# Kernel tuning notes

Measured on AMD Instinct MI355X. Metric: run time of the kernel, lower is better.

## Reference

```python
import jax, jax.numpy as jnp
import numpy as np

N_NODES = 50000

def setup_inputs() -> dict:
    key = jax.random.key(0)
    ks = jax.random.split(key, 4)
    x = jax.random.normal(ks[0], (N_NODES, 64), dtype=jnp.float32)
    edge_index = jax.random.randint(ks[1], (2, 800000), 0, N_NODES, dtype=jnp.int64)
    W1 = jax.random.normal(ks[2], (64, 128), dtype=jnp.float32) * (1.0 / np.sqrt(64))
    b1 = jnp.zeros((128,), dtype=jnp.float32)
    W2 = jax.random.normal(ks[3], (128, 64), dtype=jnp.float32) * (1.0 / np.sqrt(128))
    b2 = jnp.zeros((64,), dtype=jnp.float32)
    eps = jnp.zeros((1,), dtype=jnp.float32)
    return {"x": x, "edge_index": edge_index, "W1": W1, "b1": b1, "W2": W2, "b2": b2, "eps": eps}

def reference(x, edge_index, W1, b1, W2, b2, eps):
    row, col = edge_index[0], edge_index[1]
    # gather neighbor features [E, d] and scatter-add into destination nodes [N, d]
    agg = jax.ops.segment_sum(x[col], row, num_segments=x.shape[0])
    h = (1.0 + eps[0]) * x + agg
    # 2-layer MLP: Linear -> ReLU -> Linear
    h = jax.nn.relu(h @ W1 + b1)
    return h @ W2 + b2
```

## Files before the change

### kernel.cpp

```cpp
#include <hip/hip_runtime.h>

#define N_NODES 50000
#define N_EDGES 800000
#define D 64
#define H 128
#define NB512 128
#define NLIVE 98
#define CAP 9216
#define BT 2048
#define NBB 391
#define TILE2 2304
#define NSUB 32
#define SCAP2 352
#define CVB 798

typedef __attribute__((ext_vector_type(8))) short  short8;
typedef __attribute__((ext_vector_type(4))) float  floatx4;
typedef __attribute__((ext_vector_type(4))) unsigned short ushort4v;

__device__ inline unsigned short f2bf(float f) {
    unsigned u = __builtin_bit_cast(unsigned, f);
    u += 0x7FFFu + ((u >> 16) & 1u);
    return (unsigned short)(u >> 16);
}
__device__ inline float bf2f(unsigned short b) {
    unsigned u = (unsigned)b << 16;
    return __builtin_bit_cast(float, u);
}

__global__ __launch_bounds__(1024) void bin_prep(
    const int* __restrict__ row, const int* __restrict__ col,
    int* __restrict__ cursor, int* __restrict__ csr,
    const float* __restrict__ x, unsigned short* __restrict__ xb,
    const float* __restrict__ W1, unsigned short* __restrict__ w1t,
    const float* __restrict__ W2, unsigned short* __restrict__ w2t)
{
    int t = threadIdx.x;
    if (blockIdx.x >= NBB) {
        int tid = (blockIdx.x - NBB) * 1024 + t;
        if (tid < 800000) {
            float4 v = ((const float4*)x)[tid];
            ushort4v o;
            o.x = f2bf(v.x); o.y = f2bf(v.y); o.z = f2bf(v.z); o.w = f2bf(v.w);
            ((ushort4v*)xb)[tid] = o;
        } else {
            int i = tid - 800000;
            if (i < D * H) {
                int k = i >> 7, n = i & 127;
                w1t[n * D + k] = f2bf(W1[i]);
            } else if (i < 2 * D * H) {
                int j = i - D * H;
                int k = j >> 6, n = j & 63;
                w2t[n * H + k] = f2bf(W2[j]);
            }
        }
        return;
    }

    __shared__ int cnt[NB512];
    __shared__ int loffs[NB512];
    __shared__ int gbase[NB512];
    __shared__ int sorted[BT];
    __shared__ int wsum[2];

    int lane = t & 63;
    if (t < NB512) cnt[t] = 0;
    __syncthreads();

    int base = blockIdx.x * BT;
    int ia = base + t, ib = ia + 1024;
    int ca = min(ia, N_EDGES - 1), cb = min(ib, N_EDGES - 1);
    unsigned ra = (unsigned)row[ca], rb = (unsigned)row[cb];
    unsigned ka = (unsigned)col[ca], kb = (unsigned)col[cb];
    bool va = ia < N_EDGES, vb = ib < N_EDGES;
    if (va) atomicAdd(&cnt[ra >> 9], 1);
    if (vb) atomicAdd(&cnt[rb >> 9], 1);
    __syncthreads();

    int v = 0, incl = 0;
    if (t < NB512) {
        v = cnt[t];
        incl = v;
        #pragma unroll
        for (int d = 1; d < 64; d <<= 1) {
            int y = __shfl_up(incl, d);
            if (lane >= d) incl += y;
        }
        if (lane == 63) wsum[t >> 6] = incl;
    }
    __syncthreads();
    if (t < NB512) {
        int add = (t >= 64) ? wsum[0] : 0;
        loffs[t] = incl - v + add;
        if (v) gbase[t] = t * CAP + atomicAdd(&cursor[t], v);
    }
    __syncthreads();

    if (t < NB512) cnt[t] = 0;
    __syncthreads();

    if (va) { int b = (int)(ra >> 9); int lp = atomicAdd(&cnt[b], 1);
              sorted[loffs[b] + lp] = (int)((ra << 16) | ka); }
    if (vb) { int b = (int)(rb >> 9); int lp = atomicAdd(&cnt[b], 1);
              sorted[loffs[b] + lp] = (int)((rb << 16) | kb); }
    __syncthreads();

    int nloc = min(BT, N_EDGES - base);
    for (int i = t; i < nloc; i += 1024) {
        unsigned en = (unsigned)sorted[i];
        int b = (int)(en >> 25);
        int pos = gbase[b] + (i - loffs[b]);
        csr[pos] = (int)en;
    }
}

__global__ __launch_bounds__(256) void subsort(
    const int* __restrict__ cursor, const int* __restrict__ csr,
    int* __restrict__ cursor2, int* __restrict__ csr2)
{
    __shared__ int sorted[TILE2];
    __shared__ int cnt32[32], loffs[32], gbase[32], curs[32];

    int t = threadIdx.x, lane = t & 63;
    int bucket = blockIdx.x >> 2;
    int tile   = blockIdx.x & 3;

    int cntE = min(cursor[bucket], CAP);
    int tbeg = tile * TILE2;
    int nloc = max(min(tbeg + TILE2, cntE) - tbeg, 0);
    const int* src = csr + bucket * CAP + tbeg;

    if (t < 32) cnt32[t] = 0;
    __syncthreads();

    for (int i = t; i < nloc; i += 256)
        atomicAdd(&cnt32[(((unsigned)src[i] >> 16) & 511u) >> 4], 1);
    __syncthreads();

    if (t < 32) {
        int v = cnt32[t];
        int incl = v;
        #pragma unroll
        for (int d = 1; d < 32; d <<= 1) {
            int y = __shfl_up(incl, d);
            if (lane >= d) incl += y;
        }
        loffs[t] = incl - v;
        curs[t]  = incl - v;
        gbase[t] = v ? atomicAdd(&cursor2[bucket * 32 + t], v) : 0;
    }
    __syncthreads();

    for (int i = t; i < nloc; i += 256) {
        unsigned e = (unsigned)src[i];
        int local = (int)((e >> 16) & 511u);
        int p = atomicAdd(&curs[local >> 4], 1);
        sorted[p] = (int)(((unsigned)local << 16) | (e & 0xFFFFu));
    }
    __syncthreads();

    for (int i = t; i < nloc; i += 256) {
        unsigned en = (unsigned)sorted[i];
        int sub = (int)(en >> 20);
        int rel = gbase[sub] + (i - loffs[sub]);
        if (rel < SCAP2)
            csr2[(bucket * 32 + sub) * SCAP2 + rel] =
                (int)(((en >> 16) & 15u) << 16 | (en & 0xFFFFu));
    }
}

__global__ __launch_bounds__(256, 8) void gather_mlp(
    const float* __restrict__ x, const unsigned short* __restrict__ xb,
    const int* __restrict__ cursor2, const int* __restrict__ csr2,
    const unsigned short* __restrict__ w1t, const float* __restrict__ b1,
    const unsigned short* __restrict__ w2t, const float* __restrict__ b2,
    const float* __restrict__ eps, float* __restrict__ out)
{
    __shared__ int ent[SCAP2];
    __shared__ unsigned short scol[SCAP2];
    __shared__ int cnt16[16], offs[17], curs[16];
    __shared__ unsigned short HB[16][72];
    __shared__ unsigned short HID[16][136];

    int t = threadIdx.x, lane = t & 63, wid = t >> 6;
    int bs = blockIdx.x;
    int bucket = bs >> 5, sub = bs & 31;

    if (t < 16) cnt16[t] = 0;
    __syncthreads();

    int n2 = min(cursor2[bs], SCAP2);
    const int* src = csr2 + (size_t)bs * SCAP2;

    for (int i = t; i < n2; i += 256) {
        int e = src[i];
        ent[i] = e;
        atomicAdd(&cnt16[((unsigned)e >> 16) & 15u], 1);
    }
    __syncthreads();

    if (t < 16) {
        int v = cnt16[t];
        int incl = v;
        #pragma unroll
        for (int d = 1; d < 16; d <<= 1) {
            int y = __shfl_up(incl, d);
            if (lane >= d) incl += y;
        }
        offs[t] = incl - v;
        curs[t] = incl - v;
        if (t == 15) offs[16] = incl;
    }
    __syncthreads();

    for (int i = t; i < n2; i += 256) {
        int e = ent[i];
        int nl = (int)(((unsigned)e >> 16) & 15u);
        int p = atomicAdd(&curs[nl], 1);
        scol[p] = (unsigned short)(e & 0xFFFF);
    }
    __syncthreads();

    float ep = 1.0f + eps[0];
    int half = lane >> 5, fl = lane & 31;
    #pragma unroll 1
    for (int nn = 0; nn < 4; ++nn) {
        int nl = wid * 4 + nn;
        int node = bucket * 512 + sub * 16 + nl;
        int jb = offs[nl], je = offs[nl + 1];
        float s0a = 0.f, s1a = 0.f, s0b = 0.f, s1b = 0.f;
        float s0c = 0.f, s1c = 0.f, s0d = 0.f, s1d = 0.f;
        int j = jb;
        for (; j + 8 <= je; j += 8) {
            int c0 = scol[j + half];
            int c1 = scol[j + 2 + half];
            int c2 = scol[j + 4 + half];
            int c3 = scol[j + 6 + half];
            ushort2 p0 = *(const ushort2*)&xb[c0 * D + 2 * fl];
            ushort2 p1 = *(const ushort2*)&xb[c1 * D + 2 * fl];
            ushort2 p2 = *(const ushort2*)&xb[c2 * D + 2 * fl];
            ushort2 p3 = *(const ushort2*)&xb[c3 * D + 2 * fl];
            s0a += bf2f(p0.x); s1a += bf2f(p0.y);
            s0b += bf2f(p1.x); s1b += bf2f(p1.y);
            s0c += bf2f(p2.x); s1c += bf2f(p2.y);
            s0d += bf2f(p3.x); s1d += bf2f(p3.y);
        }
        for (; j < je; j += 2) {
            if (j + half < je) {
                int c = scol[j + half];
                ushort2 p = *(const ushort2*)&xb[c * D + 2 * fl];
                s0a += bf2f(p.x); s1a += bf2f(p.y);
            }
        }
        float s0 = (s0a + s0b) + (s0c + s0d);
        float s1 = (s1a + s1b) + (s1c + s1d);
        s0 += __shfl_xor(s0, 32);
        s1 += __shfl_xor(s1, 32);
        if (half == 0) {
            float2 xv = {0.f, 0.f};
            if (node < N_NODES) xv = *(const float2*)&x[(size_t)node * D + 2 * fl];
            ushort2 o;
            o.x = f2bf(fmaf(ep, xv.x, s0));
            o.y = f2bf(fmaf(ep, xv.y, s1));
            *(ushort2*)&HB[nl][2 * fl] = o;
        }
    }
    __syncthreads();

    if (wid == 0) {
        int m = lane & 15, q = lane >> 4;
        short8 a0 = *(const short8*)&HB[m][q * 8];
        short8 a1 = *(const short8*)&HB[m][32 + q * 8];

        #pragma unroll
        for (int nt = 0; nt < 8; ++nt) {
            float bias = b1[nt * 16 + m];
            floatx4 acc = {bias, bias, bias, bias};
            short8 w0 = *(const short8*)&w1t[(nt * 16 + m) * D + q * 8];
            short8 w1 = *(const short8*)&w1t[(nt * 16 + m) * D + 32 + q * 8];
            acc = __builtin_amdgcn_mfma_f32_16x16x32_bf16(a0, w0, acc, 0, 0, 0);
            acc = __builtin_amdgcn_mfma_f32_16x16x32_bf16(a1, w1, acc, 0, 0, 0);
            #pragma unroll
            for (int r = 0; r < 4; ++r) {
                float hv = fmaxf(acc[r], 0.0f);
                HID[q * 4 + r][nt * 16 + m] = f2bf(hv);
            }
        }

        short8 ha[4];
        #pragma unroll
        for (int kc2 = 0; kc2 < 4; ++kc2)
            ha[kc2] = *(const short8*)&HID[m][kc2 * 32 + q * 8];

        #pragma unroll
        for (int nt2 = 0; nt2 < 4; ++nt2) {
            float bias = b2[nt2 * 16 + m];
            floatx4 acc = {bias, bias, bias, bias};
            #pragma unroll
            for (int kc2 = 0; kc2 < 4; ++kc2) {
                short8 w = *(const short8*)&w2t[(nt2 * 16 + m) * H + kc2 * 32 + q * 8];
                acc = __builtin_amdgcn_mfma_f32_16x16x32_bf16(ha[kc2], w, acc, 0, 0, 0);
            }
            #pragma unroll
            for (int r = 0; r < 4; ++r) {
                int nn2 = bucket * 512 + sub * 16 + q * 4 + r;
                if (nn2 < N_NODES) out[(size_t)nn2 * D + nt2 * 16 + m] = acc[r];
            }
        }
    }
}

extern "C" void kernel_launch(void* const* d_in, const int* in_sizes, int n_in,
                              void* d_out, int out_size, void* d_ws, size_t ws_size,
                              hipStream_t stream) {
    const float* x   = (const float*)d_in[0];
    const int*   ei  = (const int*)  d_in[1];
    const float* W1  = (const float*)d_in[2];
    const float* b1  = (const float*)d_in[3];
    const float* W2  = (const float*)d_in[4];
    const float* b2  = (const float*)d_in[5];
    const float* eps = (const float*)d_in[6];
    float* out = (float*)d_out;

    unsigned short* xb  = (unsigned short*)d_ws;
    unsigned short* w1t = xb + (size_t)N_NODES * D;
    unsigned short* w2t = w1t + D * H;
    int* csr     = (int*)(w2t + D * H);
    int* csr2    = csr + (size_t)NB512 * CAP;
    int* cursor  = csr2 + (size_t)NLIVE * 32 * SCAP2;
    int* cursor2 = cursor + NB512;

    const int* row = ei;
    const int* col = ei + N_EDGES;

    hipMemsetAsync(cursor, 0, (size_t)(NB512 + NLIVE * 32) * sizeof(int), stream);
    bin_prep<<<NBB + CVB, 1024, 0, stream>>>(row, col, cursor, csr,
                                             x, xb, W1, w1t, W2, w2t);
    subsort<<<NLIVE * 4, 256, 0, stream>>>(cursor, csr, cursor2, csr2);
    gather_mlp<<<NLIVE * 32, 256, 0, stream>>>(x, xb, cursor2, csr2,
                                               w1t, b1, w2t, b2, eps, out);
}
```

Measured before the change: 128.0 us.

## Replace global bucket atomics with per-tile fixed-slot bins and drop memset

The first binning pass no longer reserves space with global atomics on per-bucket cursors. Each input tile now writes its edges into a fixed-capacity slot per bucket (52 entries) and records per-tile counts. The subsort kernel gathers these slots for its bucket across 49 tiles, and runs with 8 blocks per bucket instead of 4. The cursor2 zeroing moves into bin_prep, removing the separate memset launch. The cost is a strided, sparse gather in subsort and silent truncation if any tile/bucket pair exceeds its slot capacity.

```diff
diff --git a/kernel.cpp b/kernel.cpp
--- a/kernel.cpp
+++ b/kernel.cpp
@@ -4,13 +4,13 @@
 #define N_EDGES 800000
 #define D 64
 #define H 128
-#define NB512 128
 #define NLIVE 98
-#define CAP 9216
+#define NBPAD 128
 #define BT 2048
 #define NBB 391
-#define TILE2 2304
-#define NSUB 32
+#define CAPT 52
+#define NT8 49
+#define STG 1280
 #define SCAP2 352
 #define CVB 798
 
@@ -30,14 +30,18 @@
 
 __global__ __launch_bounds__(1024) void bin_prep(
     const int* __restrict__ row, const int* __restrict__ col,
-    int* __restrict__ cursor, int* __restrict__ csr,
+    int* __restrict__ counts, int* __restrict__ csr,
+    int* __restrict__ cursor2,
     const float* __restrict__ x, unsigned short* __restrict__ xb,
     const float* __restrict__ W1, unsigned short* __restrict__ w1t,
     const float* __restrict__ W2, unsigned short* __restrict__ w2t)
 {
     int t = threadIdx.x;
     if (blockIdx.x >= NBB) {
-        int tid = (blockIdx.x - NBB) * 1024 + t;
+        int cb = blockIdx.x - NBB;
+        if (cb == 0)
+            for (int i = t; i < NLIVE * 32; i += 1024) cursor2[i] = 0;
+        int tid = cb * 1024 + t;
         if (tid < 800000) {
             float4 v = ((const float4*)x)[tid];
             ushort4v o;
@@ -57,28 +61,27 @@
         return;
     }
 
-    __shared__ int cnt[NB512];
-    __shared__ int loffs[NB512];
-    __shared__ int gbase[NB512];
+    __shared__ int cnt[NBPAD];
+    __shared__ int loffs[NBPAD];
     __shared__ int sorted[BT];
     __shared__ int wsum[2];
 
     int lane = t & 63;
-    if (t < NB512) cnt[t] = 0;
+    if (t < NBPAD) cnt[t] = 0;
     __syncthreads();
 
     int base = blockIdx.x * BT;
     int ia = base + t, ib = ia + 1024;
-    int ca = min(ia, N_EDGES - 1), cb = min(ib, N_EDGES - 1);
-    unsigned ra = (unsigned)row[ca], rb = (unsigned)row[cb];
-    unsigned ka = (unsigned)col[ca], kb = (unsigned)col[cb];
+    int ca = min(ia, N_EDGES - 1), cb2 = min(ib, N_EDGES - 1);
+    unsigned ra = (unsigned)row[ca], rb = (unsigned)row[cb2];
+    unsigned ka = (unsigned)col[ca], kb = (unsigned)col[cb2];
     bool va = ia < N_EDGES, vb = ib < N_EDGES;
     if (va) atomicAdd(&cnt[ra >> 9], 1);
     if (vb) atomicAdd(&cnt[rb >> 9], 1);
     __syncthreads();
 
     int v = 0, incl = 0;
-    if (t < NB512) {
+    if (t < NBPAD) {
         v = cnt[t];
         incl = v;
         #pragma unroll
@@ -89,14 +92,13 @@
         if (lane == 63) wsum[t >> 6] = incl;
     }
     __syncthreads();
-    if (t < NB512) {
-        int add = (t >= 64) ? wsum[0] : 0;
-        loffs[t] = incl - v + add;
-        if (v) gbase[t] = t * CAP + atomicAdd(&cursor[t], v);
-    }
-    __syncthreads();
-
-    if (t < NB512) cnt[t] = 0;
+    if (t < NBPAD) {
+        loffs[t] = incl - v + ((t >= 64) ? wsum[0] : 0);
+        if (t < NLIVE) counts[blockIdx.x * NLIVE + t] = min(v, CAPT);
+    }
+    __syncthreads();
+
+    if (t < NBPAD) cnt[t] = 0;
     __syncthreads();
 
     if (va) { int b = (int)(ra >> 9); int lp = atomicAdd(&cnt[b], 1);
@@ -109,34 +111,44 @@
     for (int i = t; i < nloc; i += 1024) {
         unsigned en = (unsigned)sorted[i];
         int b = (int)(en >> 25);
-        int pos = gbase[b] + (i - loffs[b]);
-        csr[pos] = (int)en;
-    }
-}
-
-__global__ __launch_bounds__(256) void subsort(
-    const int* __restrict__ cursor, const int* __restrict__ csr,
+        int rel = i - loffs[b];
+        if (rel < CAPT)
+            csr[((size_t)blockIdx.x * NLIVE + b) * CAPT + rel] = (int)en;
+    }
+}
+
+__global__ __launch_bounds__(256, 8) void subsort(
+    const int* __restrict__ counts, const int* __restrict__ csr,
     int* __restrict__ cursor2, int* __restrict__ csr2)
 {
-    __shared__ int sorted[TILE2];
+    __shared__ int tcnt[NT8];
+    __shared__ int stage[STG];
+    __shared__ int sorted2[STG];
     __shared__ int cnt32[32], loffs[32], gbase[32], curs[32];
+    __shared__ int nstage;
 
     int t = threadIdx.x, lane = t & 63;
-    int bucket = blockIdx.x >> 2;
-    int tile   = blockIdx.x & 3;
-
-    int cntE = min(cursor[bucket], CAP);
-    int tbeg = tile * TILE2;
-    int nloc = max(min(tbeg + TILE2, cntE) - tbeg, 0);
-    const int* src = csr + bucket * CAP + tbeg;
+    int bucket = blockIdx.x >> 3, q = blockIdx.x & 7;
+    int tbeg = q * NT8;
+    int ntile = min(NT8, NBB - tbeg);
 
     if (t < 32) cnt32[t] = 0;
-    __syncthreads();
-
-    for (int i = t; i < nloc; i += 256)
-        atomicAdd(&cnt32[(((unsigned)src[i] >> 16) & 511u) >> 4], 1);
-    __syncthreads();
-
+    if (t == 0) nstage = 0;
+    if (t < ntile) tcnt[t] = counts[(size_t)(tbeg + t) * NLIVE + bucket];
+    __syncthreads();
+
+    for (int s = t; s < ntile * CAPT; s += 256) {
+        int tl = s / CAPT, slot = s - tl * CAPT;
+        if (slot < tcnt[tl]) {
+            int e = csr[((size_t)(tbeg + tl) * NLIVE + bucket) * CAPT + slot];
+            int p = atomicAdd(&nstage, 1);
+            stage[min(p, STG - 1)] = e;
+            atomicAdd(&cnt32[((unsigned)e >> 20) & 31u], 1);
+        }
+    }
+    __syncthreads();
+
+    int nst = min(nstage, STG);
     if (t < 32) {
         int v = cnt32[t];
         int incl = v;
@@ -151,21 +163,21 @@
     }
     __syncthreads();
 
-    for (int i = t; i < nloc; i += 256) {
-        unsigned e = (unsigned)src[i];
-        int local = (int)((e >> 16) & 511u);
-        int p = atomicAdd(&curs[local >> 4], 1);
-        sorted[p] = (int)(((unsigned)local << 16) | (e & 0xFFFFu));
-    }
-    __syncthreads();
-
-    for (int i = t; i < nloc; i += 256) {
-        unsigned en = (unsigned)sorted[i];
-        int sub = (int)(en >> 20);
+    for (int i = t; i < nst; i += 256) {
+        int e = stage[i];
+        int sub = (int)(((unsigned)e >> 20) & 31u);
+        int p = atomicAdd(&curs[sub], 1);
+        sorted2[min(p, STG - 1)] = e;
+    }
+    __syncthreads();
+
+    for (int i = t; i < nst; i += 256) {
+        unsigned en = (unsigned)sorted2[i];
+        int sub = (int)((en >> 20) & 31u);
         int rel = gbase[sub] + (i - loffs[sub]);
         if (rel < SCAP2)
-            csr2[(bucket * 32 + sub) * SCAP2 + rel] =
-                (int)(((en >> 16) & 15u) << 16 | (en & 0xFFFFu));
+            csr2[((size_t)bucket * 32 + sub) * SCAP2 + rel] =
+                (int)(en & 0xFFFFFu);
     }
 }
 
@@ -326,17 +338,16 @@
     unsigned short* w1t = xb + (size_t)N_NODES * D;
     unsigned short* w2t = w1t + D * H;
     int* csr     = (int*)(w2t + D * H);
-    int* csr2    = csr + (size_t)NB512 * CAP;
-    int* cursor  = csr2 + (size_t)NLIVE * 32 * SCAP2;
-    int* cursor2 = cursor + NB512;
+    int* counts  = csr + (size_t)NBB * NLIVE * CAPT;
+    int* csr2    = counts + (size_t)NBB * NLIVE;
+    int* cursor2 = csr2 + (size_t)NLIVE * 32 * SCAP2;
 
     const int* row = ei;
     const int* col = ei + N_EDGES;
 
-    hipMemsetAsync(cursor, 0, (size_t)(NB512 + NLIVE * 32) * sizeof(int), stream);
-    bin_prep<<<NBB + CVB, 1024, 0, stream>>>(row, col, cursor, csr,
+    bin_prep<<<NBB + CVB, 1024, 0, stream>>>(row, col, counts, csr, cursor2,
                                              x, xb, W1, w1t, W2, w2t);
-    subsort<<<NLIVE * 4, 256, 0, stream>>>(cursor, csr, cursor2, csr2);
+    subsort<<<NLIVE * 8, 256, 0, stream>>>(counts, csr, cursor2, csr2);
     gather_mlp<<<NLIVE * 32, 256, 0, stream>>>(x, xb, cursor2, csr2,
                                                w1t, b1, w2t, b2, eps, out);
 }
```

Result: faster. 121.6 us (-5.0%).
